# Performance work log

Hardware: AMD Instinct MI355X
Metric: run time of the kernel (lower is better)

Reference implementation:

```python
import jax, jax.numpy as jnp
import numpy as np

N_NODES = 100000
HIDDEN = 256
HALF = HIDDEN // 2
N_EDGES = 1000000


def setup_inputs() -> dict:
    key = jax.random.key(0)
    k1, k2 = jax.random.split(key)
    x = jax.random.normal(k1, (N_NODES, HIDDEN), dtype=jnp.float32)
    edge_label_index = jax.random.randint(k2, (2, N_EDGES), 0, N_NODES, dtype=jnp.int64)
    return {"x": x, "edge_label_index": edge_label_index}


def reference(x, edge_label_index):
    # Gather source-half features for src nodes and target-half for dst nodes,
    # per-edge dot product, sigmoid. Output shape [E, 1] as in the torch module.
    src = x[edge_label_index[0], :HALF]          # [E, HALF]
    dst = x[edge_label_index[1], HALF:]          # [E, HALF]
    logits = jnp.einsum('ed,ed->e', src, dst)    # per-edge dot
    return jax.nn.sigmoid(logits).reshape(-1, 1)
```

## Files before the change

kernel.cpp:

```cpp
#include <hip/hip_runtime.h>
#include <hip/hip_bf16.h>
#include <math.h>


#define HIDDEN 256
#define HALF   128

typedef _Float16 half8 __attribute__((ext_vector_type(8)));

__global__ __launch_bounds__(256) void cvt_fp16_kernel(
    const float* __restrict__ x, _Float16* __restrict__ y, int n16)
{
    int i = blockIdx.x * blockDim.x + threadIdx.x;
    if (i >= n16) return;
    const float4* p = (const float4*)x + (size_t)4 * i;
    float4 a = p[0];
    float4 b = p[1];
    float4 c = p[2];
    float4 d = p[3];
    half8 h0, h1;
    h0[0] = (_Float16)a.x; h0[1] = (_Float16)a.y;
    h0[2] = (_Float16)a.z; h0[3] = (_Float16)a.w;
    h0[4] = (_Float16)b.x; h0[5] = (_Float16)b.y;
    h0[6] = (_Float16)b.z; h0[7] = (_Float16)b.w;
    h1[0] = (_Float16)c.x; h1[1] = (_Float16)c.y;
    h1[2] = (_Float16)c.z; h1[3] = (_Float16)c.w;
    h1[4] = (_Float16)d.x; h1[5] = (_Float16)d.y;
    h1[6] = (_Float16)d.z; h1[7] = (_Float16)d.w;
    half8* q = (half8*)y + (size_t)2 * i;
    q[0] = h0;
    q[1] = h1;
}

__global__ __launch_bounds__(256) void decoder_fp16_kernel(
    const _Float16* __restrict__ y,
    const int* __restrict__ eidx,
    float* __restrict__ out,
    int n_edges)
{
    int tid   = blockIdx.x * blockDim.x + threadIdx.x;
    int group = tid >> 4;
    int lane  = tid & 15;
    int e0 = group * 2;
    if (e0 >= n_edges) return;
    bool has2 = (e0 + 1) < n_edges;
    int e1 = has2 ? (e0 + 1) : e0;

    int s0 = eidx[e0];
    int d0 = eidx[n_edges + e0];
    int s1 = eidx[e1];
    int d1 = eidx[n_edges + e1];

    half8 a0 = ((const half8*)(y + (size_t)s0 * HIDDEN))[lane];
    half8 b0 = ((const half8*)(y + (size_t)d0 * HIDDEN + HALF))[lane];
    half8 a1 = ((const half8*)(y + (size_t)s1 * HIDDEN))[lane];
    half8 b1 = ((const half8*)(y + (size_t)d1 * HIDDEN + HALF))[lane];

    float acc0 = 0.f, acc1 = 0.f;
    #pragma unroll
    for (int j = 0; j < 8; ++j) {
        acc0 += (float)a0[j] * (float)b0[j];
        acc1 += (float)a1[j] * (float)b1[j];
    }

    #pragma unroll
    for (int off = 8; off > 0; off >>= 1) {
        acc0 += __shfl_down(acc0, off, 16);
        acc1 += __shfl_down(acc1, off, 16);
    }

    if (lane == 0) {
        float r0 = 1.0f / (1.0f + __expf(-acc0));
        float r1 = 1.0f / (1.0f + __expf(-acc1));
        if (has2) {
            ((float2*)out)[group] = make_float2(r0, r1);
        } else {
            out[e0] = r0;
        }
    }
}

__global__ __launch_bounds__(256) void decoder_fp32_kernel(
    const float* __restrict__ x,
    const int* __restrict__ eidx,
    float* __restrict__ out,
    int n_edges)
{
    int tid  = blockIdx.x * blockDim.x + threadIdx.x;
    int edge = tid >> 5;
    int lane = tid & 31;
    if (edge >= n_edges) return;

    int s = eidx[edge];
    int d = eidx[n_edges + edge];

    const float4* sp = (const float4*)(x + (size_t)s * HIDDEN) + lane;
    const float4* dp = (const float4*)(x + (size_t)d * HIDDEN + HALF) + lane;

    float4 a = *sp;
    float4 b = *dp;
    float acc = a.x * b.x + a.y * b.y + a.z * b.z + a.w * b.w;

    #pragma unroll
    for (int off = 16; off > 0; off >>= 1)
        acc += __shfl_down(acc, off, 32);

    if (lane == 0) {
        out[edge] = 1.0f / (1.0f + __expf(-acc));
    }
}

extern "C" void kernel_launch(void* const* d_in, const int* in_sizes, int n_in,
                              void* d_out, int out_size, void* d_ws, size_t ws_size,
                              hipStream_t stream)
{
    const float* x    = (const float*)d_in[0];
    const int*   eidx = (const int*)d_in[1];
    float*       out  = (float*)d_out;

    int n_edges  = out_size;
    int n_elems  = in_sizes[0];
    size_t need  = (size_t)n_elems * 2;

    if (ws_size >= need) {
        _Float16* y = (_Float16*)d_ws;

        int n16 = n_elems / 16;
        cvt_fp16_kernel<<<(n16 + 255) / 256, 256, 0, stream>>>(x, y, n16);

        const int threads = 256;
        int groups = (n_edges + 1) / 2;
        int total  = groups * 16;
        int blocks = (total + threads - 1) / threads;
        decoder_fp16_kernel<<<blocks, threads, 0, stream>>>(y, eidx, out, n_edges);
    } else {
        const int threads = 256;
        const int epb = threads / 32;
        int blocks = (n_edges + epb - 1) / epb;
        decoder_fp32_kernel<<<blocks, threads, 0, stream>>>(x, eidx, out, n_edges);
    }
}
```

Baseline: 222.3 us.

## Fuse fp16 conversion and edge decoder into one cooperative persistent kernel

```diff
diff --git a/kernel.cpp b/kernel.cpp
--- a/kernel.cpp
+++ b/kernel.cpp
@@ -1,5 +1,5 @@
 #include <hip/hip_runtime.h>
-#include <hip/hip_bf16.h>
+#include <hip/hip_cooperative_groups.h>
 #include <math.h>
 
 
@@ -7,29 +7,98 @@
 #define HALF   128
 
 typedef _Float16 half8 __attribute__((ext_vector_type(8)));
+typedef _Float16 half4 __attribute__((ext_vector_type(4)));
+typedef _Float16 half2_t __attribute__((ext_vector_type(2)));
+
+namespace cg = cooperative_groups;
+
+__device__ __forceinline__ float dot8(half8 a, half8 b)
+{
+    float acc = 0.f;
+    #pragma unroll
+    for (int j = 0; j < 4; ++j) {
+        half2_t aj = { a[2*j], a[2*j+1] };
+        half2_t bj = { b[2*j], b[2*j+1] };
+        acc = __builtin_amdgcn_fdot2(aj, bj, acc, false);
+    }
+    return acc;
+}
+
+__global__ __launch_bounds__(256, 8) void fused_decoder_kernel(
+    const float* __restrict__ x,
+    const int* __restrict__ eidx,
+    float* __restrict__ out,
+    _Float16* __restrict__ y,
+    int n4, int n_edges)
+{
+    int t = blockIdx.x * blockDim.x + threadIdx.x;
+    int nthreads = gridDim.x * blockDim.x;
+
+    const float4* x4 = (const float4*)x;
+    half4* y4 = (half4*)y;
+    for (int i = t; i < n4; i += nthreads) {
+        float4 v = x4[i];
+        half4 h;
+        h[0] = (_Float16)v.x; h[1] = (_Float16)v.y;
+        h[2] = (_Float16)v.z; h[3] = (_Float16)v.w;
+        y4[i] = h;
+    }
+
+    cg::this_grid().sync();
+
+    int lane = t & 15;
+    int group0 = t >> 4;
+    int gstride = nthreads >> 4;
+    int total_groups = (n_edges + 1) >> 1;
+
+    for (int g = group0; g < total_groups; g += gstride) {
+        int e0 = g << 1;
+        bool has2 = (e0 + 1) < n_edges;
+        int e1 = has2 ? e0 + 1 : e0;
+
+        int s0 = eidx[e0];
+        int d0 = eidx[n_edges + e0];
+        int s1 = eidx[e1];
+        int d1 = eidx[n_edges + e1];
+
+        half8 a0 = ((const half8*)(y + (size_t)s0 * HIDDEN))[lane];
+        half8 b0 = ((const half8*)(y + (size_t)d0 * HIDDEN + HALF))[lane];
+        half8 a1 = ((const half8*)(y + (size_t)s1 * HIDDEN))[lane];
+        half8 b1 = ((const half8*)(y + (size_t)d1 * HIDDEN + HALF))[lane];
+
+        float acc0 = dot8(a0, b0);
+        float acc1 = dot8(a1, b1);
+
+        #pragma unroll
+        for (int off = 8; off > 0; off >>= 1) {
+            acc0 += __shfl_down(acc0, off, 16);
+            acc1 += __shfl_down(acc1, off, 16);
+        }
+
+        if (lane == 0) {
+            float r0 = 1.0f / (1.0f + __expf(-acc0));
+            float r1 = 1.0f / (1.0f + __expf(-acc1));
+            if (has2) ((float2*)out)[g] = make_float2(r0, r1);
+            else      out[e0] = r0;
+        }
+    }
+}
+
 
 __global__ __launch_bounds__(256) void cvt_fp16_kernel(
-    const float* __restrict__ x, _Float16* __restrict__ y, int n16)
-{
-    int i = blockIdx.x * blockDim.x + threadIdx.x;
-    if (i >= n16) return;
-    const float4* p = (const float4*)x + (size_t)4 * i;
-    float4 a = p[0];
-    float4 b = p[1];
-    float4 c = p[2];
-    float4 d = p[3];
-    half8 h0, h1;
-    h0[0] = (_Float16)a.x; h0[1] = (_Float16)a.y;
-    h0[2] = (_Float16)a.z; h0[3] = (_Float16)a.w;
-    h0[4] = (_Float16)b.x; h0[5] = (_Float16)b.y;
-    h0[6] = (_Float16)b.z; h0[7] = (_Float16)b.w;
-    h1[0] = (_Float16)c.x; h1[1] = (_Float16)c.y;
-    h1[2] = (_Float16)c.z; h1[3] = (_Float16)c.w;
-    h1[4] = (_Float16)d.x; h1[5] = (_Float16)d.y;
-    h1[6] = (_Float16)d.z; h1[7] = (_Float16)d.w;
-    half8* q = (half8*)y + (size_t)2 * i;
-    q[0] = h0;
-    q[1] = h1;
+    const float* __restrict__ x, _Float16* __restrict__ y, int n4)
+{
+    int t = blockIdx.x * blockDim.x + threadIdx.x;
+    int stride = gridDim.x * blockDim.x;
+    const float4* x4 = (const float4*)x;
+    half4* y4 = (half4*)y;
+    for (int i = t; i < n4; i += stride) {
+        float4 v = x4[i];
+        half4 h;
+        h[0] = (_Float16)v.x; h[1] = (_Float16)v.y;
+        h[2] = (_Float16)v.z; h[3] = (_Float16)v.w;
+        y4[i] = h;
+    }
 }
 
 __global__ __launch_bounds__(256) void decoder_fp16_kernel(
@@ -56,12 +125,8 @@
     half8 a1 = ((const half8*)(y + (size_t)s1 * HIDDEN))[lane];
     half8 b1 = ((const half8*)(y + (size_t)d1 * HIDDEN + HALF))[lane];
 
-    float acc0 = 0.f, acc1 = 0.f;
-    #pragma unroll
-    for (int j = 0; j < 8; ++j) {
-        acc0 += (float)a0[j] * (float)b0[j];
-        acc1 += (float)a1[j] * (float)b1[j];
-    }
+    float acc0 = dot8(a0, b0);
+    float acc1 = dot8(a1, b1);
 
     #pragma unroll
     for (int off = 8; off > 0; off >>= 1) {
@@ -72,11 +137,8 @@
     if (lane == 0) {
         float r0 = 1.0f / (1.0f + __expf(-acc0));
         float r1 = 1.0f / (1.0f + __expf(-acc1));
-        if (has2) {
-            ((float2*)out)[group] = make_float2(r0, r1);
-        } else {
-            out[e0] = r0;
-        }
+        if (has2) ((float2*)out)[group] = make_float2(r0, r1);
+        else      out[e0] = r0;
     }
 }
 
@@ -118,25 +180,36 @@
     const int*   eidx = (const int*)d_in[1];
     float*       out  = (float*)d_out;
 
-    int n_edges  = out_size;
-    int n_elems  = in_sizes[0];
-    size_t need  = (size_t)n_elems * 2;
+    int n_edges = out_size;
+    int n_elems = in_sizes[0];
+    size_t need = (size_t)n_elems * 2;
 
     if (ws_size >= need) {
         _Float16* y = (_Float16*)d_ws;
-
-        int n16 = n_elems / 16;
-        cvt_fp16_kernel<<<(n16 + 255) / 256, 256, 0, stream>>>(x, y, n16);
-
-        const int threads = 256;
+        int n4 = n_elems / 4;
+
+        int maxb = 0;
+        hipError_t qerr = hipOccupancyMaxActiveBlocksPerMultiprocessor(
+            &maxb, fused_decoder_kernel, 256, 0);
+
+        if (qerr == hipSuccess && maxb > 0) {
+            int grid = maxb * 256;
+            if (grid > 2048) grid = 2048;
+            void* args[] = { (void*)&x, (void*)&eidx, (void*)&out,
+                             (void*)&y, (void*)&n4, (void*)&n_edges };
+            hipError_t lerr = hipLaunchCooperativeKernel(
+                (void*)fused_decoder_kernel, dim3(grid), dim3(256), args, 0, stream);
+            if (lerr == hipSuccess) return;
+        }
+
+        cvt_fp16_kernel<<<2048, 256, 0, stream>>>(x, y, n4);
         int groups = (n_edges + 1) / 2;
-        int total  = groups * 16;
-        int blocks = (total + threads - 1) / threads;
-        decoder_fp16_kernel<<<blocks, threads, 0, stream>>>(y, eidx, out, n_edges);
+        long long total = (long long)groups * 16;
+        int blocks = (int)((total + 255) / 256);
+        decoder_fp16_kernel<<<blocks, 256, 0, stream>>>(y, eidx, out, n_edges);
     } else {
-        const int threads = 256;
-        const int epb = threads / 32;
-        int blocks = (n_edges + epb - 1) / epb;
-        decoder_fp32_kernel<<<blocks, threads, 0, stream>>>(x, eidx, out, n_edges);
-    }
-}
+        int blocks = (n_edges * 32 + 255) / 256 / 1;
+        blocks = (n_edges + 7) / 8;
+        decoder_fp32_kernel<<<blocks, 256, 0, stream>>>(x, eidx, out, n_edges);
+    }
+}
```

New measurement: 370.1 us. +66.5%, slower.
